# Performance work log

Hardware: AMD Instinct MI355X
Metric: run time of the kernel (lower is better)

Reference implementation:

```python
import jax, jax.numpy as jnp
import numpy as np

N_NODES = 100000
N_EDGES = 1600000
NODE_DIM = 3
EDGE_DIM = 32
HIDDEN = 128
OUT_DIM = 3
N_GRAPHS = 64


def _lin(key, fan_in, fan_out):
    k1, k2 = jax.random.split(key)
    s = 1.0 / np.sqrt(fan_in)
    W = jax.random.uniform(k1, (fan_in, fan_out), minval=-s, maxval=s, dtype=jnp.float32)
    b = jax.random.uniform(k2, (fan_out,), minval=-s, maxval=s, dtype=jnp.float32)
    return W, b


def setup_inputs() -> dict:
    key = jax.random.key(0)
    ks = jax.random.split(key, 16)
    x = jax.random.normal(ks[0], (N_NODES, NODE_DIM), dtype=jnp.float32)
    edge_index = jax.random.randint(ks[1], (2, N_EDGES), 0, N_NODES, dtype=jnp.int32)
    edge_attr = jax.random.normal(ks[2], (N_EDGES, EDGE_DIM), dtype=jnp.float32)
    batch = jnp.sort(jax.random.randint(ks[3], (N_NODES,), 0, N_GRAPHS, dtype=jnp.int32))
    # conv1: CGConv at channels=NODE_DIM, in = 2*NODE_DIM + EDGE_DIM
    Wf1, bf1 = _lin(ks[4], 2 * NODE_DIM + EDGE_DIM, NODE_DIM)
    Ws1, bs1 = _lin(ks[5], 2 * NODE_DIM + EDGE_DIM, NODE_DIM)
    Wp, bp = _lin(ks[6], NODE_DIM, HIDDEN)
    # two hidden CGConvs at channels=HIDDEN
    Wf2, bf2 = _lin(ks[7], 2 * HIDDEN + EDGE_DIM, HIDDEN)
    Ws2, bs2 = _lin(ks[8], 2 * HIDDEN + EDGE_DIM, HIDDEN)
    Wf3, bf3 = _lin(ks[9], 2 * HIDDEN + EDGE_DIM, HIDDEN)
    Ws3, bs3 = _lin(ks[10], 2 * HIDDEN + EDGE_DIM, HIDDEN)
    W1, b1 = _lin(ks[11], HIDDEN, HIDDEN)
    W2, b2 = _lin(ks[12], HIDDEN, OUT_DIM)
    return dict(x=x, edge_index=edge_index, edge_attr=edge_attr, batch=batch,
                Wf1=Wf1, bf1=bf1, Ws1=Ws1, bs1=bs1, Wp=Wp, bp=bp,
                Wf2=Wf2, bf2=bf2, Ws2=Ws2, bs2=bs2,
                Wf3=Wf3, bf3=bf3, Ws3=Ws3, bs3=bs3,
                W1=W1, b1=b1, W2=W2, b2=b2)


def _cgconv(x, src, dst, edge_attr, Wf, bf, Ws, bs):
    # z = [x_i (target), x_j (source), e_ij]; message = sigmoid(lin_f(z)) * softplus(lin_s(z))
    z = jnp.concatenate([x[dst], x[src], edge_attr], axis=-1)  # [E, 2C+F]
    m = jax.nn.sigmoid(z @ Wf + bf) * jax.nn.softplus(z @ Ws + bs)  # [E, C]
    agg = jax.ops.segment_sum(m, dst, num_segments=x.shape[0])
    return x + agg


def reference(x, edge_index, edge_attr, batch,
              Wf1, bf1, Ws1, bs1, Wp, bp,
              Wf2, bf2, Ws2, bs2, Wf3, bf3, Ws3, bs3,
              W1, b1, W2, b2):
    src, dst = edge_index[0], edge_index[1]
    h = _cgconv(x, src, dst, edge_attr, Wf1, bf1, Ws1, bs1)
    h = jax.nn.relu(h @ Wp + bp)
    h = jax.nn.relu(_cgconv(h, src, dst, edge_attr, Wf2, bf2, Ws2, bs2))
    h = jax.nn.relu(_cgconv(h, src, dst, edge_attr, Wf3, bf3, Ws3, bs3))
    # global mean pool over graphs
    sums = jax.ops.segment_sum(h, batch, num_segments=N_GRAPHS)
    counts = jax.ops.segment_sum(jnp.ones((h.shape[0],), h.dtype), batch, num_segments=N_GRAPHS)
    pooled = sums / jnp.maximum(counts, 1.0)[:, None]
    g = jax.nn.relu(pooled @ W1 + b1)
    return g @ W2 + b2
```

## Files before the change

kernel.cpp:

```cpp
#include <hip/hip_runtime.h>
#include <hip/hip_bf16.h>


#define N_NODES 100000
#define N_EDGES 1600000
#define HID 128
#define SCAN_BLOCKS 391

typedef unsigned int uint;
typedef unsigned long long ull;
typedef short bf16x8 __attribute__((ext_vector_type(8)));
typedef float f32x4 __attribute__((ext_vector_type(4)));

__device__ inline float bflo(uint u) { return __uint_as_float(u << 16); }
__device__ inline float bfhi(uint u) { return __uint_as_float(u & 0xffff0000u); }
__device__ inline uint pack_bf16_2(float a, float b) {
  uint ua = __float_as_uint(a), ub = __float_as_uint(b);
  ua = (ua + 0x7fffu + ((ua >> 16) & 1u)) >> 16;
  ub = (ub + 0x7fffu + ((ub >> 16) & 1u)) >> 16;
  return ua | (ub << 16);
}
__device__ inline float sigmoidf_(float x) {
  return __builtin_amdgcn_rcpf(1.f + __expf(-x));
}
__device__ inline float softplusf_(float x) {
  return fmaxf(x, 0.f) + __logf(1.f + __expf(-fabsf(x)));
}

__global__ __launch_bounds__(256) void hist_k(const int* __restrict__ ei,
                                              int* __restrict__ deg) {
  int e = blockIdx.x * 256 + threadIdx.x;
  if (e >= N_EDGES) return;
  atomicAdd(&deg[ei[N_EDGES + e]], 1);
}

__global__ __launch_bounds__(256) void scan1_k(const int* __restrict__ deg,
                                               int* __restrict__ rowptr,
                                               int* __restrict__ bsums) {
  __shared__ int s[256];
  int i = blockIdx.x * 256 + threadIdx.x;
  int v = (i < N_NODES) ? deg[i] : 0;
  s[threadIdx.x] = v;
  __syncthreads();
  for (int off = 1; off < 256; off <<= 1) {
    int t = (threadIdx.x >= off) ? s[threadIdx.x - off] : 0;
    __syncthreads();
    s[threadIdx.x] += t;
    __syncthreads();
  }
  if (i < N_NODES) rowptr[i] = s[threadIdx.x] - v;
  if (threadIdx.x == 255) bsums[blockIdx.x] = s[255];
}

__global__ __launch_bounds__(512) void scan2_k(int* __restrict__ bsums) {
  __shared__ int s[512];
  int t = threadIdx.x;
  int v = (t < SCAN_BLOCKS) ? bsums[t] : 0;
  s[t] = v;
  __syncthreads();
  for (int off = 1; off < 512; off <<= 1) {
    int x = (t >= off) ? s[t - off] : 0;
    __syncthreads();
    s[t] += x;
    __syncthreads();
  }
  if (t < SCAN_BLOCKS) bsums[t] = s[t] - v;
}

__global__ __launch_bounds__(256) void scan3_k(int* __restrict__ rowptr,
                                               const int* __restrict__ bsums,
                                               int* __restrict__ cur) {
  int i = blockIdx.x * 256 + threadIdx.x;
  if (i < N_NODES) {
    int r = rowptr[i] + bsums[blockIdx.x];
    rowptr[i] = r;
    cur[i] = r;
  }
  if (i == 0) rowptr[N_NODES] = N_EDGES;
}

__global__ __launch_bounds__(256) void scatter_k(const int* __restrict__ ei,
                                                 int* __restrict__ cur,
                                                 uint4* __restrict__ csr) {
  int e = blockIdx.x * 256 + threadIdx.x;
  if (e >= N_EDGES) return;
  int d = ei[N_EDGES + e];
  int pos = atomicAdd(&cur[d], 1);
  csr[pos] = make_uint4((uint)ei[e], (uint)e, (uint)d, 0u);
}

__global__ __launch_bounds__(256) void ea_pack(const float* __restrict__ ea,
                                               const uint4* __restrict__ csr,
                                               uint4* __restrict__ eab) {
  long long t = (long long)blockIdx.x * 256 + threadIdx.x;
  int p = (int)(t >> 2), q = (int)(t & 3);
  if (p >= N_EDGES) return;
  uint e = csr[p].y;
  const float4* er = (const float4*)(ea + (long long)e * 32 + q * 8);
  float4 a0 = er[0], a1 = er[1];
  uint4 pk;
  pk.x = pack_bf16_2(a0.x, a0.y);
  pk.y = pack_bf16_2(a0.z, a0.w);
  pk.z = pack_bf16_2(a1.x, a1.y);
  pk.w = pack_bf16_2(a1.z, a1.w);
  eab[(long long)p * 4 + q] = pk;
}

__global__ __launch_bounds__(256) void conv1_edge(
    const float* __restrict__ x, const int* __restrict__ ei,
    const float* __restrict__ ea,
    const float* __restrict__ Wf, const float* __restrict__ bf,
    const float* __restrict__ Ws, const float* __restrict__ bs,
    float* __restrict__ agg1) {
  int e = blockIdx.x * 256 + threadIdx.x;
  if (e >= N_EDGES) return;
  int src = ei[e], dst = ei[N_EDGES + e];
  float z[38];
#pragma unroll
  for (int k = 0; k < 3; ++k) z[k] = x[dst * 3 + k];
#pragma unroll
  for (int k = 0; k < 3; ++k) z[3 + k] = x[src * 3 + k];
  const float4* er4 = (const float4*)(ea + (long long)e * 32);
#pragma unroll
  for (int k = 0; k < 8; ++k) {
    float4 v = er4[k];
    z[6 + 4 * k + 0] = v.x;
    z[6 + 4 * k + 1] = v.y;
    z[6 + 4 * k + 2] = v.z;
    z[6 + 4 * k + 3] = v.w;
  }
#pragma unroll
  for (int c = 0; c < 3; ++c) {
    float f = bf[c], s = bs[c];
#pragma unroll
    for (int k = 0; k < 38; ++k) {
      f = fmaf(z[k], Wf[k * 3 + c], f);
      s = fmaf(z[k], Ws[k * 3 + c], s);
    }
    atomicAdd(&agg1[dst * 3 + c], sigmoidf_(f) * softplusf_(s));
  }
}

__global__ __launch_bounds__(256) void proj2(
    const float* __restrict__ x, const float* __restrict__ agg1,
    const float* __restrict__ Wp, const float* __restrict__ bp,
    float* __restrict__ h, uint* __restrict__ hb) {
  long long i = (long long)blockIdx.x * 256 + threadIdx.x;
  if (i >= (long long)N_NODES * 64) return;
  int n = (int)(i >> 6), jp = (int)(i & 63);
  int j0 = jp * 2;
  float v0 = x[n * 3 + 0] + agg1[n * 3 + 0];
  float v1 = x[n * 3 + 1] + agg1[n * 3 + 1];
  float v2 = x[n * 3 + 2] + agg1[n * 3 + 2];
  float a0 = bp[j0], a1 = bp[j0 + 1];
  a0 = fmaf(v0, Wp[0 * HID + j0], a0);
  a0 = fmaf(v1, Wp[1 * HID + j0], a0);
  a0 = fmaf(v2, Wp[2 * HID + j0], a0);
  a1 = fmaf(v0, Wp[0 * HID + j0 + 1], a1);
  a1 = fmaf(v1, Wp[1 * HID + j0 + 1], a1);
  a1 = fmaf(v2, Wp[2 * HID + j0 + 1], a1);
  a0 = fmaxf(a0, 0.f);
  a1 = fmaxf(a1, 0.f);
  *(float2*)&h[(long long)n * HID + j0] = make_float2(a0, a1);
  hb[(long long)n * 64 + jp] = pack_bf16_2(a0, a1);
}

__global__ __launch_bounds__(256) void w_prep2(const float* __restrict__ Wf,
                                               const float* __restrict__ Ws,
                                               uint* __restrict__ Wpk) {
  int row = blockIdx.x * 256 + threadIdx.x;
  int pm = row >> 7;
  int c = row & 127;
  const float* W = (pm & 1) ? Ws : Wf;
  int rowoff = (pm >> 1) * 128;
  for (int kk = 0; kk < 64; ++kk) {
    float a = W[(rowoff + 2 * kk) * 128 + c];
    float b = W[(rowoff + 2 * kk + 1) * 128 + c];
    Wpk[row * 64 + kk] = pack_bf16_2(a, b);
  }
}

#define NG_STR 68
__global__ __launch_bounds__(256, 4) void node_gemmM(
    const uint* __restrict__ hb, const uint* __restrict__ Wpk,
    const float* __restrict__ bf, const float* __restrict__ bs,
    uint* __restrict__ Pb) {
  __shared__ uint Alds[64 * NG_STR];
  int part = blockIdx.x;
  int m0 = blockIdx.y * 64;
  int tid = threadIdx.x;
  {
    int r = tid >> 2, q = tid & 3;
    int row = m0 + r;
    uint* d = &Alds[r * NG_STR + q * 16];
    if (row < N_NODES) {
      const uint4* s4 = (const uint4*)&hb[(long long)row * 64 + q * 16];
      uint4 v0 = s4[0], v1 = s4[1], v2 = s4[2], v3 = s4[3];
      *(uint4*)(d + 0) = v0; *(uint4*)(d + 4) = v1;
      *(uint4*)(d + 8) = v2; *(uint4*)(d + 12) = v3;
    } else {
      uint4 z = make_uint4(0, 0, 0, 0);
      *(uint4*)(d + 0) = z; *(uint4*)(d + 4) = z;
      *(uint4*)(d + 8) = z; *(uint4*)(d + 12) = z;
    }
  }
  __syncthreads();
  int wave = tid >> 6, lane = tid & 63;
  int l15 = lane & 15, lq = lane >> 4;
  int arow = wave * 16 + l15;
  const uint* WpF = Wpk + (part * 2 + 0) * 128 * 64;
  const uint* WpS = Wpk + (part * 2 + 1) * 128 * 64;
  f32x4 accF[8], accS[8];
#pragma unroll
  for (int nt = 0; nt < 8; ++nt) {
    f32x4 z = {0.f, 0.f, 0.f, 0.f};
    accF[nt] = z;
    accS[nt] = z;
  }
#pragma unroll
  for (int ks = 0; ks < 4; ++ks) {
    bf16x8 afr = *(const bf16x8*)&Alds[arow * NG_STR + ks * 16 + lq * 4];
#pragma unroll
    for (int nt = 0; nt < 8; ++nt) {
      bf16x8 bF = *(const bf16x8*)&WpF[(nt * 16 + l15) * 64 + ks * 16 + lq * 4];
      bf16x8 bS = *(const bf16x8*)&WpS[(nt * 16 + l15) * 64 + ks * 16 + lq * 4];
      accF[nt] = __builtin_amdgcn_mfma_f32_16x16x32_bf16(afr, bF, accF[nt], 0, 0, 0);
      accS[nt] = __builtin_amdgcn_mfma_f32_16x16x32_bf16(afr, bS, accS[nt], 0, 0, 0);
    }
  }
#pragma unroll
  for (int nt = 0; nt < 8; ++nt) {
    int c = nt * 16 + l15;
    int pos = (nt >> 1) * 32 + l15 * 2 + (nt & 1);
    float fb = (part == 0) ? bf[c] : 0.f;
    float sb = (part == 0) ? bs[c] : 0.f;
#pragma unroll
    for (int reg = 0; reg < 4; ++reg) {
      int node = m0 + wave * 16 + lq * 4 + reg;
      if (node < N_NODES) {
        Pb[(long long)node * 256 + part * 128 + pos] =
            pack_bf16_2(accF[nt][reg] + fb, accS[nt][reg] + sb);
      }
    }
  }
}

__global__ __launch_bounds__(256) void w_prep(const float* __restrict__ Wf,
                                              const float* __restrict__ Ws,
                                              uint* __restrict__ Btg) {
  int t = threadIdx.x;
  const float* W = (t < 128) ? Wf : Ws;
  int c = t & 127;
#pragma unroll
  for (int kk = 0; kk < 16; ++kk) {
    float a = W[(256 + 2 * kk) * 128 + c];
    float b = W[(256 + 2 * kk + 1) * 128 + c];
    Btg[t * 16 + kk] = pack_bf16_2(a, b);
  }
}

#define EMSG_EB 128
#define CAP 24
__global__ __launch_bounds__(256, 7) void edge_msg(
    const uint* __restrict__ Pb, const uint* __restrict__ eab,
    const uint* __restrict__ Btg, const uint4* __restrict__ csr,
    const int* __restrict__ rowptr, float* __restrict__ h) {
  __shared__ float accL[CAP * 128];
  __shared__ int dstL[EMSG_EB], srcL[EMSG_EB], liL[EMSG_EB];
  __shared__ int dlist[CAP], compL[CAP];
  __shared__ int nDistS, wcnt0S;
  int tid = threadIdx.x;
  int j0 = blockIdx.x * EMSG_EB;
#pragma unroll
  for (int i = 0; i < (CAP * 128) / 256; ++i) accL[tid + i * 256] = 0.f;
  int li_me = -1, d_me = 0;
  bool flag = false;
  ull mball = 0;
  if (tid < EMSG_EB) {
    uint4 cj = csr[j0 + tid];
    d_me = (int)cj.z;
    dstL[tid] = d_me;
    srcL[tid] = (int)cj.x;
    int l = tid & 63;
    int dp = __shfl_up(d_me, 1, 64);
    int dprev = (l == 0) ? ((tid == 0) ? -1 : (int)csr[j0 + tid - 1].z) : dp;
    flag = (d_me != dprev);
    mball = __ballot(flag);
    ull pre = (l == 63) ? ~0ull : ((1ull << (l + 1)) - 1);
    li_me = __popcll(mball & pre) - 1;
    if (tid == 0) wcnt0S = __popcll(mball);
  }
  __syncthreads();
  if (tid >= 64 && tid < EMSG_EB) li_me += wcnt0S;
  if (tid < EMSG_EB) {
    liL[tid] = li_me;
    if (flag && li_me < CAP) {
      dlist[li_me] = d_me;
      int r0 = rowptr[d_me], r1 = rowptr[d_me + 1];
      compL[li_me] = ((r0 == j0 + tid) && (r1 <= j0 + EMSG_EB)) ? 1 : 0;
    }
    if (tid == 64) nDistS = wcnt0S + __popcll(mball);
  }
  __syncthreads();
  int wave = tid >> 6, lane = tid & 63;
  int c0w = wave * 32;
  int l15 = lane & 15, lq = lane >> 4;
  int chs0 = c0w + l15, chs1 = c0w + 16 + l15;
  int pbase = (wave << 5) + (l15 << 1);
  bf16x8 bfr0 = *(const bf16x8*)&Btg[chs0 * 16 + lq * 4];
  bf16x8 bfr1 = *(const bf16x8*)&Btg[chs1 * 16 + lq * 4];
  bf16x8 bfr2 = *(const bf16x8*)&Btg[(128 + chs0) * 16 + lq * 4];
  bf16x8 bfr3 = *(const bf16x8*)&Btg[(128 + chs1) * 16 + lq * 4];
#pragma unroll
  for (int mt = 0; mt < 8; ++mt) {
    bf16x8 afr =
        *(const bf16x8*)&eab[((long long)(j0 + mt * 16 + l15)) * 16 + lq * 4];
    f32x4 z = {0.f, 0.f, 0.f, 0.f};
    f32x4 accf0 = __builtin_amdgcn_mfma_f32_16x16x32_bf16(afr, bfr0, z, 0, 0, 0);
    f32x4 accf1 = __builtin_amdgcn_mfma_f32_16x16x32_bf16(afr, bfr1, z, 0, 0, 0);
    f32x4 accs0 = __builtin_amdgcn_mfma_f32_16x16x32_bf16(afr, bfr2, z, 0, 0, 0);
    f32x4 accs1 = __builtin_amdgcn_mfma_f32_16x16x32_bf16(afr, bfr3, z, 0, 0, 0);
    int o = mt * 16 + lq * 4;
    int dsts[4], lis[4];
#pragma unroll
    for (int reg = 0; reg < 4; ++reg) {
      dsts[reg] = dstL[o + reg];
      lis[reg] = liL[o + reg];
    }
    float mr0[4], mr1[4];
#pragma unroll
    for (int reg = 0; reg < 4; ++reg) {
      uint2 gd = *(const uint2*)&Pb[(long long)dsts[reg] * 256 + pbase];
      uint2 gs = *(const uint2*)&Pb[(long long)srcL[o + reg] * 256 + 128 + pbase];
      float f0 = accf0[reg] + bflo(gd.x) + bflo(gs.x);
      float s0 = accs0[reg] + bfhi(gd.x) + bfhi(gs.x);
      float f1 = accf1[reg] + bflo(gd.y) + bflo(gs.y);
      float s1 = accs1[reg] + bfhi(gd.y) + bfhi(gs.y);
      mr0[reg] = sigmoidf_(f0) * softplusf_(s0);
      mr1[reg] = sigmoidf_(f1) * softplusf_(s1);
    }
#pragma unroll
    for (int cp = 0; cp < 2; ++cp) {
      int c = (cp ? chs1 : chs0);
      const float* mr = cp ? mr1 : mr0;
      float racc = mr[0];
      int cl = lis[0], cd = dsts[0];
#pragma unroll
      for (int reg = 1; reg < 4; ++reg) {
        if (lis[reg] == cl) {
          racc += mr[reg];
        } else {
          if (cl < CAP) atomicAdd(&accL[cl * 128 + c], racc);
          else atomicAdd(&h[(long long)cd * HID + c], racc);
          cl = lis[reg]; cd = dsts[reg]; racc = mr[reg];
        }
      }
      if (cl < CAP) atomicAdd(&accL[cl * 128 + c], racc);
      else atomicAdd(&h[(long long)cd * HID + c], racc);
    }
  }
  __syncthreads();
  int nD = nDistS;
  if (nD > CAP) nD = CAP;
  int c = tid & 127;
  for (int li = tid >> 7; li < nD; li += 2) {
    int d = dlist[li];
    float v = accL[li * 128 + c];
    float* hp = &h[(long long)d * HID + c];
    if (compL[li]) {
      *hp = fmaxf(*hp + v, 0.f);
    } else {
      atomicAdd(hp, v);
    }
  }
}

__global__ __launch_bounds__(256) void relu2(float* __restrict__ h,
                                             uint* __restrict__ hb) {
  const int total = N_NODES * 32;
  for (int i = blockIdx.x * 256 + threadIdx.x; i < total; i += gridDim.x * 256) {
    float4 v = ((float4*)h)[i];
    v.x = fmaxf(v.x, 0.f); v.y = fmaxf(v.y, 0.f);
    v.z = fmaxf(v.z, 0.f); v.w = fmaxf(v.w, 0.f);
    ((float4*)h)[i] = v;
    uint2 o;
    o.x = pack_bf16_2(v.x, v.y);
    o.y = pack_bf16_2(v.z, v.w);
    *(uint2*)&hb[(long long)i * 2] = o;
  }
}

__global__ __launch_bounds__(256) void relu_k(float* __restrict__ h) {
  const int total = N_NODES * HID / 4;
  for (int i = blockIdx.x * 256 + threadIdx.x; i < total; i += gridDim.x * 256) {
    float4 v = ((float4*)h)[i];
    v.x = fmaxf(v.x, 0.f); v.y = fmaxf(v.y, 0.f);
    v.z = fmaxf(v.z, 0.f); v.w = fmaxf(v.w, 0.f);
    ((float4*)h)[i] = v;
  }
}

#define POOL_NODES 32
__global__ __launch_bounds__(128) void pool2(
    const float* __restrict__ h, const int* __restrict__ batch,
    float* __restrict__ sums, float* __restrict__ cnts) {
  int n0 = blockIdx.x * POOL_NODES;
  if (n0 >= N_NODES) return;
  int t = threadIdx.x;
  int nEnd = n0 + POOL_NODES;
  if (nEnd > N_NODES) nEnd = N_NODES;
  float acc = 0.f;
  int bcur = batch[n0];
  int cnt = 0;
  for (int n = n0; n < nEnd; ++n) {
    int b = batch[n];
    if (b != bcur) {
      atomicAdd(&sums[bcur * HID + t], acc);
      if (t == 0) atomicAdd(&cnts[bcur], (float)cnt);
      acc = 0.f; cnt = 0; bcur = b;
    }
    acc += h[(long long)n * HID + t];
    ++cnt;
  }
  atomicAdd(&sums[bcur * HID + t], acc);
  if (t == 0) atomicAdd(&cnts[bcur], (float)cnt);
}

__global__ __launch_bounds__(128) void mlpA(
    const float* __restrict__ sums, const float* __restrict__ cnts,
    const float* __restrict__ W1, const float* __restrict__ b1,
    float* __restrict__ g) {
  __shared__ float pl[HID];
  int gr = blockIdx.x, j = threadIdx.x;
  float cnt = fmaxf(cnts[gr], 1.f);
  pl[j] = sums[gr * HID + j] / cnt;
  __syncthreads();
  float acc = b1[j];
#pragma unroll 8
  for (int k = 0; k < HID; ++k) acc = fmaf(pl[k], W1[k * HID + j], acc);
  g[gr * HID + j] = fmaxf(acc, 0.f);
}

__global__ __launch_bounds__(256) void mlpB(
    const float* __restrict__ g, const float* __restrict__ W2,
    const float* __restrict__ b2, float* __restrict__ out) {
  int t = threadIdx.x;
  if (t >= 64 * 3) return;
  int gr = t / 3, o = t % 3;
  float acc = b2[o];
#pragma unroll 8
  for (int k = 0; k < HID; ++k) acc = fmaf(g[gr * HID + k], W2[k * 3 + o], acc);
  out[t] = acc;
}

extern "C" void kernel_launch(void* const* d_in, const int* in_sizes, int n_in,
                              void* d_out, int out_size, void* d_ws, size_t ws_size,
                              hipStream_t stream) {
  const float* x   = (const float*)d_in[0];
  const int*   ei  = (const int*)d_in[1];
  const float* ea  = (const float*)d_in[2];
  const int*   bat = (const int*)d_in[3];
  const float* Wf1 = (const float*)d_in[4];
  const float* bf1 = (const float*)d_in[5];
  const float* Ws1 = (const float*)d_in[6];
  const float* bs1 = (const float*)d_in[7];
  const float* Wp  = (const float*)d_in[8];
  const float* bp  = (const float*)d_in[9];
  const float* Wf2 = (const float*)d_in[10];
  const float* bf2 = (const float*)d_in[11];
  const float* Ws2 = (const float*)d_in[12];
  const float* bs2 = (const float*)d_in[13];
  const float* Wf3 = (const float*)d_in[14];
  const float* bf3 = (const float*)d_in[15];
  const float* Ws3 = (const float*)d_in[16];
  const float* bs3 = (const float*)d_in[17];
  const float* W1  = (const float*)d_in[18];
  const float* b1  = (const float*)d_in[19];
  const float* W2  = (const float*)d_in[20];
  const float* b2  = (const float*)d_in[21];
  float* out = (float*)d_out;

  char* w = (char*)d_ws;
  size_t off = 0;
  auto alloc = [&](size_t bytes) {
    void* p = w + off;
    off += (bytes + 255) & ~(size_t)255;
    return p;
  };
  int*   deg    = (int*)alloc((size_t)N_NODES * 4);
  int*   rowptr = (int*)alloc((size_t)(N_NODES + 1) * 4);
  int*   cur    = (int*)alloc((size_t)N_NODES * 4);
  int*   bsums  = (int*)alloc((size_t)512 * 4);
  uint4* csr    = (uint4*)alloc((size_t)N_EDGES * 16);
  float* agg1   = (float*)alloc((size_t)N_NODES * 3 * 4);
  float* h      = (float*)alloc((size_t)N_NODES * HID * 4);
  uint*  hb     = (uint*)alloc((size_t)N_NODES * 64 * 4);
  uint*  Pb     = (uint*)alloc((size_t)N_NODES * 256 * 4);
  uint*  eab    = (uint*)alloc((size_t)N_EDGES * 64);
  float* sums   = (float*)alloc((size_t)64 * HID * 4);
  float* cnts   = (float*)alloc((size_t)64 * 4);
  float* g      = (float*)alloc((size_t)64 * HID * 4);
  uint*  Btg    = (uint*)alloc((size_t)256 * 16 * 4);
  uint*  Wpk    = (uint*)alloc((size_t)512 * 64 * 4);
  (void)ws_size;

  hipMemsetAsync(deg, 0, (size_t)N_NODES * 4, stream);
  hist_k<<<(N_EDGES + 255) / 256, 256, 0, stream>>>(ei, deg);
  scan1_k<<<SCAN_BLOCKS, 256, 0, stream>>>(deg, rowptr, bsums);
  scan2_k<<<1, 512, 0, stream>>>(bsums);
  scan3_k<<<SCAN_BLOCKS, 256, 0, stream>>>(rowptr, bsums, cur);
  scatter_k<<<(N_EDGES + 255) / 256, 256, 0, stream>>>(ei, cur, csr);
  ea_pack<<<(N_EDGES * 4 + 255) / 256, 256, 0, stream>>>(ea, csr, (uint4*)eab);

  hipMemsetAsync(agg1, 0, (size_t)N_NODES * 3 * 4, stream);
  conv1_edge<<<(N_EDGES + 255) / 256, 256, 0, stream>>>(x, ei, ea, Wf1, bf1, Ws1, bs1, agg1);
  proj2<<<(N_NODES * 64 + 255) / 256, 256, 0, stream>>>(x, agg1, Wp, bp, h, hb);

  dim3 nggrid(2, (N_NODES + 63) / 64);
  int eblocks = N_EDGES / EMSG_EB;

  w_prep2<<<2, 256, 0, stream>>>(Wf2, Ws2, Wpk);
  node_gemmM<<<nggrid, 256, 0, stream>>>(hb, Wpk, bf2, bs2, Pb);
  w_prep<<<1, 256, 0, stream>>>(Wf2, Ws2, Btg);
  edge_msg<<<eblocks, 256, 0, stream>>>(Pb, eab, Btg, csr, rowptr, h);
  relu2<<<4096, 256, 0, stream>>>(h, hb);

  w_prep2<<<2, 256, 0, stream>>>(Wf3, Ws3, Wpk);
  node_gemmM<<<nggrid, 256, 0, stream>>>(hb, Wpk, bf3, bs3, Pb);
  w_prep<<<1, 256, 0, stream>>>(Wf3, Ws3, Btg);
  edge_msg<<<eblocks, 256, 0, stream>>>(Pb, eab, Btg, csr, rowptr, h);
  relu_k<<<4096, 256, 0, stream>>>(h);

  hipMemsetAsync(sums, 0, (size_t)(64 * HID + 64) * 4, stream);
  pool2<<<(N_NODES + POOL_NODES - 1) / POOL_NODES, 128, 0, stream>>>(h, bat, sums, cnts);
  mlpA<<<64, 128, 0, stream>>>(sums, cnts, W1, b1, g);
  mlpB<<<1, 256, 0, stream>>>(g, W2, b2, out);
}
```

Baseline: 1.882 ms.

## Merge weight-prep kernels, stage dst rows in LDS, fold final ReLU into pool

Merges the two weight-packing kernels into one launch per layer. node_gemmM now writes packed F/S results as 8-byte stores instead of 4-byte ones. edge_msg preloads each block's first 16 distinct destination node rows of Pb into LDS so per-edge destination gathers read shared memory instead of global. The standalone final ReLU pass is dropped and applied inside the pool reduction. Together these cut launch count, global traffic and one full pass over h, at the cost of extra LDS use and an added barrier in edge_msg, which may lower occupancy.

```diff
diff --git a/kernel.cpp b/kernel.cpp
--- a/kernel.cpp
+++ b/kernel.cpp
@@ -165,18 +165,31 @@
   hb[(long long)n * 64 + jp] = pack_bf16_2(a0, a1);
 }
 
-__global__ __launch_bounds__(256) void w_prep2(const float* __restrict__ Wf,
-                                               const float* __restrict__ Ws,
-                                               uint* __restrict__ Wpk) {
-  int row = blockIdx.x * 256 + threadIdx.x;
-  int pm = row >> 7;
-  int c = row & 127;
-  const float* W = (pm & 1) ? Ws : Wf;
-  int rowoff = (pm >> 1) * 128;
-  for (int kk = 0; kk < 64; ++kk) {
-    float a = W[(rowoff + 2 * kk) * 128 + c];
-    float b = W[(rowoff + 2 * kk + 1) * 128 + c];
-    Wpk[row * 64 + kk] = pack_bf16_2(a, b);
+__global__ __launch_bounds__(256) void w_prepAll(const float* __restrict__ Wf,
+                                                 const float* __restrict__ Ws,
+                                                 uint* __restrict__ Wpk,
+                                                 uint* __restrict__ Btg) {
+  int gid = blockIdx.x * 256 + threadIdx.x;
+  if (gid < 512) {
+    int pm = gid >> 7;
+    int c = gid & 127;
+    const float* W = (pm & 1) ? Ws : Wf;
+    int rowoff = (pm >> 1) * 128;
+    for (int kk = 0; kk < 64; ++kk) {
+      float a = W[(rowoff + 2 * kk) * 128 + c];
+      float b = W[(rowoff + 2 * kk + 1) * 128 + c];
+      Wpk[gid * 64 + kk] = pack_bf16_2(a, b);
+    }
+  } else {
+    int t = gid - 512;
+    const float* W = (t < 128) ? Wf : Ws;
+    int c = t & 127;
+#pragma unroll
+    for (int kk = 0; kk < 16; ++kk) {
+      float a = W[(256 + 2 * kk) * 128 + c];
+      float b = W[(256 + 2 * kk + 1) * 128 + c];
+      Btg[t * 16 + kk] = pack_bf16_2(a, b);
+    }
   }
 }
 
@@ -229,43 +242,35 @@
     }
   }
 #pragma unroll
-  for (int nt = 0; nt < 8; ++nt) {
-    int c = nt * 16 + l15;
-    int pos = (nt >> 1) * 32 + l15 * 2 + (nt & 1);
-    float fb = (part == 0) ? bf[c] : 0.f;
-    float sb = (part == 0) ? bs[c] : 0.f;
+  for (int k = 0; k < 4; ++k) {
+    int cA = (2 * k) * 16 + l15, cB = (2 * k + 1) * 16 + l15;
+    int pos = k * 32 + l15 * 2;
+    float fbA = (part == 0) ? bf[cA] : 0.f;
+    float sbA = (part == 0) ? bs[cA] : 0.f;
+    float fbB = (part == 0) ? bf[cB] : 0.f;
+    float sbB = (part == 0) ? bs[cB] : 0.f;
 #pragma unroll
     for (int reg = 0; reg < 4; ++reg) {
       int node = m0 + wave * 16 + lq * 4 + reg;
       if (node < N_NODES) {
-        Pb[(long long)node * 256 + part * 128 + pos] =
-            pack_bf16_2(accF[nt][reg] + fb, accS[nt][reg] + sb);
+        uint2 o;
+        o.x = pack_bf16_2(accF[2 * k][reg] + fbA, accS[2 * k][reg] + sbA);
+        o.y = pack_bf16_2(accF[2 * k + 1][reg] + fbB, accS[2 * k + 1][reg] + sbB);
+        *(uint2*)&Pb[(long long)node * 256 + part * 128 + pos] = o;
       }
     }
-  }
-}
-
-__global__ __launch_bounds__(256) void w_prep(const float* __restrict__ Wf,
-                                              const float* __restrict__ Ws,
-                                              uint* __restrict__ Btg) {
-  int t = threadIdx.x;
-  const float* W = (t < 128) ? Wf : Ws;
-  int c = t & 127;
-#pragma unroll
-  for (int kk = 0; kk < 16; ++kk) {
-    float a = W[(256 + 2 * kk) * 128 + c];
-    float b = W[(256 + 2 * kk + 1) * 128 + c];
-    Btg[t * 16 + kk] = pack_bf16_2(a, b);
   }
 }
 
 #define EMSG_EB 128
 #define CAP 24
+#define GCAP 16
 __global__ __launch_bounds__(256, 7) void edge_msg(
     const uint* __restrict__ Pb, const uint* __restrict__ eab,
     const uint* __restrict__ Btg, const uint4* __restrict__ csr,
     const int* __restrict__ rowptr, float* __restrict__ h) {
   __shared__ float accL[CAP * 128];
+  __shared__ uint dgL[GCAP * 128];
   __shared__ int dstL[EMSG_EB], srcL[EMSG_EB], liL[EMSG_EB];
   __shared__ int dlist[CAP], compL[CAP];
   __shared__ int nDistS, wcnt0S;
@@ -302,6 +307,12 @@
     if (tid == 64) nDistS = wcnt0S + __popcll(mball);
   }
   __syncthreads();
+  {
+    int nG = nDistS;
+    if (nG > GCAP) nG = GCAP;
+    for (int i = tid; i < nG * 128; i += 256)
+      dgL[i] = Pb[(long long)dlist[i >> 7] * 256 + (i & 127)];
+  }
   int wave = tid >> 6, lane = tid & 63;
   int c0w = wave * 32;
   int l15 = lane & 15, lq = lane >> 4;
@@ -311,6 +322,7 @@
   bf16x8 bfr1 = *(const bf16x8*)&Btg[chs1 * 16 + lq * 4];
   bf16x8 bfr2 = *(const bf16x8*)&Btg[(128 + chs0) * 16 + lq * 4];
   bf16x8 bfr3 = *(const bf16x8*)&Btg[(128 + chs1) * 16 + lq * 4];
+  __syncthreads();
 #pragma unroll
   for (int mt = 0; mt < 8; ++mt) {
     bf16x8 afr =
@@ -330,7 +342,11 @@
     float mr0[4], mr1[4];
 #pragma unroll
     for (int reg = 0; reg < 4; ++reg) {
-      uint2 gd = *(const uint2*)&Pb[(long long)dsts[reg] * 256 + pbase];
+      uint2 gd;
+      if (lis[reg] < GCAP)
+        gd = *(const uint2*)&dgL[lis[reg] * 128 + pbase];
+      else
+        gd = *(const uint2*)&Pb[(long long)dsts[reg] * 256 + pbase];
       uint2 gs = *(const uint2*)&Pb[(long long)srcL[o + reg] * 256 + 128 + pbase];
       float f0 = accf0[reg] + bflo(gd.x) + bflo(gs.x);
       float s0 = accs0[reg] + bfhi(gd.x) + bfhi(gs.x);
@@ -387,16 +403,6 @@
     o.x = pack_bf16_2(v.x, v.y);
     o.y = pack_bf16_2(v.z, v.w);
     *(uint2*)&hb[(long long)i * 2] = o;
-  }
-}
-
-__global__ __launch_bounds__(256) void relu_k(float* __restrict__ h) {
-  const int total = N_NODES * HID / 4;
-  for (int i = blockIdx.x * 256 + threadIdx.x; i < total; i += gridDim.x * 256) {
-    float4 v = ((float4*)h)[i];
-    v.x = fmaxf(v.x, 0.f); v.y = fmaxf(v.y, 0.f);
-    v.z = fmaxf(v.z, 0.f); v.w = fmaxf(v.w, 0.f);
-    ((float4*)h)[i] = v;
   }
 }
 
@@ -419,7 +425,7 @@
       if (t == 0) atomicAdd(&cnts[bcur], (float)cnt);
       acc = 0.f; cnt = 0; bcur = b;
     }
-    acc += h[(long long)n * HID + t];
+    acc += fmaxf(h[(long long)n * HID + t], 0.f);
     ++cnt;
   }
   atomicAdd(&sums[bcur * HID + t], acc);
@@ -519,17 +525,14 @@
   dim3 nggrid(2, (N_NODES + 63) / 64);
   int eblocks = N_EDGES / EMSG_EB;
 
-  w_prep2<<<2, 256, 0, stream>>>(Wf2, Ws2, Wpk);
+  w_prepAll<<<3, 256, 0, stream>>>(Wf2, Ws2, Wpk, Btg);
   node_gemmM<<<nggrid, 256, 0, stream>>>(hb, Wpk, bf2, bs2, Pb);
-  w_prep<<<1, 256, 0, stream>>>(Wf2, Ws2, Btg);
   edge_msg<<<eblocks, 256, 0, stream>>>(Pb, eab, Btg, csr, rowptr, h);
   relu2<<<4096, 256, 0, stream>>>(h, hb);
 
-  w_prep2<<<2, 256, 0, stream>>>(Wf3, Ws3, Wpk);
+  w_prepAll<<<3, 256, 0, stream>>>(Wf3, Ws3, Wpk, Btg);
   node_gemmM<<<nggrid, 256, 0, stream>>>(hb, Wpk, bf3, bs3, Pb);
-  w_prep<<<1, 256, 0, stream>>>(Wf3, Ws3, Btg);
   edge_msg<<<eblocks, 256, 0, stream>>>(Pb, eab, Btg, csr, rowptr, h);
-  relu_k<<<4096, 256, 0, stream>>>(h);
 
   hipMemsetAsync(sums, 0, (size_t)(64 * HID + 64) * 4, stream);
   pool2<<<(N_NODES + POOL_NODES - 1) / POOL_NODES, 128, 0, stream>>>(h, bat, sums, cnts);
```

Result: slower. 1.923 ms (+2.2%).
